# Performance work log

Measured on AMD Instinct MI355X. Metric: run time of the kernel, lower is better.

## Reference

```python
import jax, jax.numpy as jnp
import numpy as np

C_IN = 512


def _rms(h, gamma):
    # F.normalize(x, dim=1) * sqrt(C) * gamma  (channel_first, h: [b, c, l])
    c = h.shape[1]
    n = jnp.sqrt(jnp.sum(h * h, axis=1, keepdims=True))
    return h / jnp.maximum(n, 1e-12) * (c ** 0.5) * gamma[None, :, None]


def _pw(w, b, h):
    # 1x1 conv == pointwise linear over channel dim; h: [b, c, l]
    return jnp.einsum('oc,bcl->bol', w, h) + b[None, :, None]


def setup_inputs() -> dict:
    key = jax.random.key(0)
    ks = jax.random.split(key, 10)
    B, C, T, H, W = 1, C_IN, 16, 32, 32
    inp = {'x': jax.random.normal(ks[0], (B, C, T, H, W), jnp.float32)}
    names = ['qs', 'ks', 'vs', 'ps', 'qt', 'kt', 'vt', 'pt']
    for i, n in enumerate(names):
        inp[n + '_w'] = jax.random.normal(ks[i + 1], (C, C), jnp.float32) * 0.02
        inp[n + '_b'] = jnp.zeros((C,), jnp.float32)
    inp['norm_s_gamma'] = jnp.ones((C,), jnp.float32)
    inp['norm_t_gamma'] = jnp.ones((C,), jnp.float32)
    inp['max_temporal_window'] = 8
    return inp


def reference(x, qs_w, qs_b, ks_w, ks_b, vs_w, vs_b, ps_w, ps_b,
              qt_w, qt_b, kt_w, kt_b, vt_w, vt_b, pt_w, pt_b,
              norm_s_gamma, norm_t_gamma, max_temporal_window):
    B, C, T, H, W = x.shape
    scale = C ** -0.5

    # ---- spatial attention: (b t) c (h w) ----
    xs = x.transpose(0, 2, 1, 3, 4).reshape(B * T, C, H * W)
    h = _rms(xs, norm_s_gamma)
    q = _pw(qs_w, qs_b, h)
    k = _pw(ks_w, ks_b, h)
    v = _pw(vs_w, vs_b, h)
    scores = jnp.einsum('bcl,bcm->blm', q, k) * scale  # [bt, HW, HW]
    attn = jax.nn.softmax(scores, axis=-1)
    o = jnp.einsum('bcm,blm->bcl', v, attn)
    xs = xs + _pw(ps_w, ps_b, o)
    x = xs.reshape(B, T, C, H, W).transpose(0, 2, 1, 3, 4)

    # ---- temporal attention: (b h w) c t, causal + bounded window ----
    xt = x.transpose(0, 3, 4, 1, 2).reshape(B * H * W, C, T)
    h = _rms(xt, norm_t_gamma)
    q = _pw(qt_w, qt_b, h)
    k = _pw(kt_w, kt_b, h)
    v = _pw(vt_w, vt_b, h)
    scores = jnp.einsum('bcl,bcm->blm', q, k) * scale  # [bhw, T, T]
    i = jnp.arange(T)[:, None]
    j = jnp.arange(T)[None, :]
    allowed = j <= i  # causal
    if max_temporal_window is not None and max_temporal_window > 0:
        allowed = allowed & (i - j < max_temporal_window)  # sliding window
    mask = jnp.where(allowed, 0.0, jnp.finfo(scores.dtype).min)
    attn = jax.nn.softmax(scores + mask[None], axis=-1)
    o = jnp.einsum('bcm,blm->bcl', v, attn)
    xt = xt + _pw(pt_w, pt_b, o)
    x = xt.reshape(B, H, W, C, T).transpose(0, 3, 4, 1, 2)
    return x
```

## Files before the change

### kernel.cpp

```cpp
#include <hip/hip_runtime.h>

typedef __attribute__((ext_vector_type(8))) short bf16x8;
typedef __attribute__((ext_vector_type(4))) float f32x4;

__device__ __forceinline__ short f2bf(float f) {
  union { float f; unsigned u; } a; a.f = f;
  unsigned r = a.u + 0x7fffu + ((a.u >> 16) & 1u);
  return (short)(r >> 16);
}
__device__ __forceinline__ float bf2f(short s) {
  union { unsigned u; float f; } a;
  a.u = ((unsigned)(unsigned short)s) << 16; return a.f;
}
__device__ __forceinline__ float blo(unsigned u) { union { unsigned u; float f; } a; a.u = u << 16; return a.f; }
__device__ __forceinline__ float bhi(unsigned u) { union { unsigned u; float f; } a; a.u = u & 0xffff0000u; return a.f; }
__device__ __forceinline__ unsigned packbf(float lo, float hi) {
  return (unsigned)(unsigned short)f2bf(lo) | ((unsigned)(unsigned short)f2bf(hi) << 16);
}
__device__ __forceinline__ void ldscp16(const void* g, void* l) {
  __builtin_amdgcn_global_load_lds((const __attribute__((address_space(1))) void*)g,
                                   (__attribute__((address_space(3))) void*)l, 16, 0, 0);
}
__device__ __forceinline__ void stv(float* p, float v) { *p = v; }
__device__ __forceinline__ void stv(short* p, float v) { *p = f2bf(v); }

__global__ __launch_bounds__(256) void setup_all(
    const float* __restrict__ w0, const float* __restrict__ w1,
    const float* __restrict__ w2, const float* __restrict__ w3,
    const float* __restrict__ w4, const float* __restrict__ w5,
    const float* __restrict__ w6, const float* __restrict__ w7,
    const float* __restrict__ g_s, const float* __restrict__ g_t,
    short* __restrict__ Wb, float* __restrict__ zs,
    const float* __restrict__ qs_b, const float* __restrict__ vs_b,
    const float* __restrict__ ps_b, const float* __restrict__ qt_b,
    const float* __restrict__ vt_b, const float* __restrict__ pt_b,
    float* __restrict__ bt_s, float* __restrict__ bt_t,
    float* __restrict__ wus, float* __restrict__ wut) {
  const int bid = blockIdx.x, tid = threadIdx.x;
  if (bid < 8192) {
    int idx = bid * 256 + tid;
    const float* ws[8] = {w0, w1, w2, w3, w4, w5, w6, w7};
    int wi = idx >> 18, loc = idx & 262143;
    int r = loc >> 9, q = loc & 511;
    float v, g;
    if (wi == 3 || wi == 7) { v = ws[wi][loc]; g = 1.f; }
    else {
      v = ws[wi][q * 512 + r];
      g = (wi <= 2) ? g_s[r] : g_t[r];
    }
    Wb[idx] = f2bf(v * g);
  } else if (bid < 8512) {
    zs[(bid - 8192) * 256 + tid] = 0.f;
  } else {
    const int w = tid >> 6, lane = tid & 63;
    const int b = (bid - 8512) * 4 + w;
    float s = 0.f;
    if (b < 1024) {
      const bool sp = b < 512;
      const float* W = sp ? w3 : w7;
      const float* vb = sp ? vs_b : vt_b;
      const int r = b & 511;
#pragma unroll
      for (int c = lane; c < 512; c += 64) s += W[r * 512 + c] * vb[c];
#pragma unroll
      for (int off = 32; off > 0; off >>= 1) s += __shfl_xor(s, off);
      if (lane == 0) (sp ? bt_s : bt_t)[r] = s + (sp ? ps_b : pt_b)[r];
    } else {
      const bool sp = b < 1536;
      const float* W = sp ? w1 : w5;
      const float* qb = sp ? qs_b : qt_b;
      const int c = b & 511;
#pragma unroll
      for (int o = lane; o < 512; o += 64) s += W[o * 512 + c] * qb[o];
#pragma unroll
      for (int off = 32; off > 0; off >>= 1) s += __shfl_xor(s, off);
      if (lane == 0)
        (sp ? wus : wut)[c] = s * (sp ? g_s[c] : g_t[c]);
    }
  }
}

__global__ __launch_bounds__(256) void txp_sumsq(
    const float* __restrict__ src, short* __restrict__ dst,
    short* __restrict__ xb, float* __restrict__ ss,
    const float* __restrict__ wu, float* __restrict__ us) {
  constexpr long N = 16384;
  __shared__ short T[64][66];
  __shared__ float part[16][16][4];
  __shared__ float part2[16][16][4];
  const int tid = threadIdx.x;
  const long n0 = (long)blockIdx.x * 64;
  const int c0 = blockIdx.y * 64;
  const int n4 = (tid & 15) * 4;
  float s0 = 0.f, s1 = 0.f, s2 = 0.f, s3 = 0.f;
  float u0 = 0.f, u1 = 0.f, u2 = 0.f, u3 = 0.f;
#pragma unroll
  for (int i = 0; i < 4; ++i) {
    int cl = i * 16 + (tid >> 4);
    float4 v = *(const float4*)&src[(long)(c0 + cl) * N + n0 + n4];
    float wc = wu[c0 + cl];
    s0 += v.x * v.x; s1 += v.y * v.y; s2 += v.z * v.z; s3 += v.w * v.w;
    u0 += wc * v.x; u1 += wc * v.y; u2 += wc * v.z; u3 += wc * v.w;
    short e0 = f2bf(v.x), e1 = f2bf(v.y), e2 = f2bf(v.z), e3 = f2bf(v.w);
    T[n4 + 0][cl] = e0; T[n4 + 1][cl] = e1;
    T[n4 + 2][cl] = e2; T[n4 + 3][cl] = e3;
    uint2 o;
    o.x = (unsigned)(unsigned short)e0 | ((unsigned)(unsigned short)e1 << 16);
    o.y = (unsigned)(unsigned short)e2 | ((unsigned)(unsigned short)e3 << 16);
    *(uint2*)&xb[(long)(c0 + cl) * N + n0 + n4] = o;
  }
  part[tid >> 4][tid & 15][0] = s0; part[tid >> 4][tid & 15][1] = s1;
  part[tid >> 4][tid & 15][2] = s2; part[tid >> 4][tid & 15][3] = s3;
  part2[tid >> 4][tid & 15][0] = u0; part2[tid >> 4][tid & 15][1] = u1;
  part2[tid >> 4][tid & 15][2] = u2; part2[tid >> 4][tid & 15][3] = u3;
  __syncthreads();
  if (tid < 64) {
    float s = 0.f, u = 0.f;
#pragma unroll
    for (int cg = 0; cg < 16; ++cg) {
      s += part[cg][tid >> 2][tid & 3];
      u += part2[cg][tid >> 2][tid & 3];
    }
    atomicAdd(&ss[n0 + tid], s);
    atomicAdd(&us[n0 + tid], u);
  }
#pragma unroll
  for (int p = 0; p < 4; ++p) {
    int nl = p * 16 + (tid >> 4);
    int cl = (tid & 15) * 4;
    uint2 o;
    o.x = (unsigned)(unsigned short)T[nl][cl] |
          ((unsigned)(unsigned short)T[nl][cl + 1] << 16);
    o.y = (unsigned)(unsigned short)T[nl][cl + 2] |
          ((unsigned)(unsigned short)T[nl][cl + 3] << 16);
    *(uint2*)&dst[(n0 + nl) * 512 + c0 + cl] = o;
  }
}

template <typename OutT, int BIAS_MODE, int SCALE_MODE, int RESID_MODE, int EPI,
          int BM = 128, int FOLD = 0, int BK = 64, int SWZ = 0>
__global__ __launch_bounds__(256, (BM == 64) ? 5 : 4) void gemm_nt(
    const short* __restrict__ A, const short* __restrict__ B,
    OutT* __restrict__ D, const float* __restrict__ bias,
    const float* __restrict__ ssv, const float* __restrict__ uvec,
    float* __restrict__ rs, float* __restrict__ rs2,
    const float* __restrict__ wvec,
    const float* __restrict__ residf, const short* __restrict__ residb,
    int K, int lda, int ldb, int ldd,
    long aBatch, long bBatch, long dBatch, long sBatch, float scale) {
  constexpr int WR = (BM >= 64) ? BM / 64 : 1;
  constexpr int WC = 4 / WR;
  constexpr int NW = (128 / WC) / 16;
  constexpr int WCS = 128 / WC;
  constexpr int CH = BK / 8;
  constexpr int MSK = CH - 1;
  constexpr int RPR = 256 / CH;
  __shared__ short As[BM * BK];
  __shared__ short Bs[128 * BK];
  const int tid = threadIdx.x;

  int lin = blockIdx.x + gridDim.x * (blockIdx.y + gridDim.y * blockIdx.z);
  if (SWZ) {
    const int nwg = gridDim.x * gridDim.y * gridDim.z;
    const int q = nwg >> 3, r = nwg & 7;
    const int xcd = lin & 7, idx = lin >> 3;
    lin = (xcd < r ? xcd * (q + 1) : r * (q + 1) + (xcd - r) * q) + idx;
  }
  const int bx = lin % gridDim.x;
  const int t1 = lin / gridDim.x;
  const int by = t1 % gridDim.y;
  const int bz = t1 / gridDim.y;

  const long i0 = (long)bx * BM;
  const long j0 = (long)by * 128;
  long aOff, bOff;
  if (FOLD) {
    aOff = 262144L * (bz < 2 ? 3 + 4 * bz : 4 * (bz - 2));
    bOff = 262144L * (bz < 2 ? 2 + 4 * bz : 1 + 4 * (bz - 2));
  } else {
    aOff = bz * aBatch; bOff = bz * bBatch;
  }
  const short* Ab = A + aOff + i0 * lda;
  const short* Bb = B + bOff + j0 * ldb;
  const int srow = tid / CH, scol = tid & MSK;
  const int lane = tid & 63;
  const int waveid = tid >> 6;
  const int wr = (waveid / WC) * 64;
  const int wc = (waveid % WC) * WCS;
  const int quad = lane >> 4, l15 = lane & 15;

  f32x4 acc[4][NW] = {};

  for (int k0 = 0; k0 < K; k0 += BK) {
    __syncthreads();
#pragma unroll
    for (int p = 0; p < BM / RPR; ++p) {
      int row = p * RPR + srow;
      int gc = (scol ^ (row & MSK)) << 3;
      ldscp16(Ab + (long)row * lda + k0 + gc, &As[p * 2048 + tid * 8]);
    }
#pragma unroll
    for (int p = 0; p < 128 / RPR; ++p) {
      int row = p * RPR + srow;
      int gc = (scol ^ (row & MSK)) << 3;
      ldscp16(Bb + (long)row * ldb + k0 + gc, &Bs[p * 2048 + tid * 8]);
    }
    __syncthreads();
#pragma unroll
    for (int kk = 0; kk < BK / 32; ++kk) {
      bf16x8 af[4], bfr[NW];
#pragma unroll
      for (int a = 0; a < 4; ++a) {
        int row = wr + a * 16 + l15;
        int g = kk * 4 + quad;
        af[a] = *(const bf16x8*)&As[row * BK + ((g ^ (row & MSK)) << 3)];
      }
#pragma unroll
      for (int b = 0; b < NW; ++b) {
        int row = wc + b * 16 + l15;
        int g = kk * 4 + quad;
        bfr[b] = *(const bf16x8*)&Bs[row * BK + ((g ^ (row & MSK)) << 3)];
      }
#pragma unroll
      for (int a = 0; a < 4; ++a)
#pragma unroll
        for (int b = 0; b < NW; ++b)
          acc[a][b] = __builtin_amdgcn_mfma_f32_16x16x32_bf16(af[a], bfr[b], acc[a][b], 0, 0, 0);
    }
  }

  const long Doff = bz * dBatch;
#pragma unroll
  for (int a = 0; a < 4; ++a) {
    const int rb = (int)i0 + wr + a * 16 + quad * 4;
    float rsc[4];
    if (SCALE_MODE == 1 || SCALE_MODE == 4) {
#pragma unroll
      for (int r = 0; r < 4; ++r)
        rsc[r] = 22.627416997969522f /
                 fmaxf(sqrtf(ssv[bz * sBatch + rb + r]), 1e-12f);
    }
    if (SCALE_MODE == 3) {
#pragma unroll
      for (int r = 0; r < 4; ++r)
        rsc[r] = 1.f / ssv[bz * sBatch + rb + r];
    }
    float rp1[4] = {0.f, 0.f, 0.f, 0.f};
    float rp2[4] = {0.f, 0.f, 0.f, 0.f};
#pragma unroll
    for (int b = 0; b < NW; ++b) {
      const int cc = (int)j0 + wc + b * 16 + l15;
      float csc = 1.f, uu = 0.f, wv = 0.f;
      if (SCALE_MODE == 2 || SCALE_MODE == 4)
        csc = 22.627416997969522f /
              fmaxf(sqrtf(ssv[bz * sBatch + cc]), 1e-12f);
      if (SCALE_MODE == 4) uu = uvec[bz * sBatch + cc];
      if (EPI == 3) wv = wvec[cc];
      uint2 rtv;
      if (RESID_MODE == 3)
        rtv = *(const uint2*)&residb[(long)cc * 512 + rb];
#pragma unroll
      for (int r = 0; r < 4; ++r) {
        float val;
        if (SCALE_MODE == 4) {
          val = __expf(scale * csc * (rsc[r] * acc[a][b][r] + uu));
          rp1[r] += val;
          val *= csc;
        } else {
          val = acc[a][b][r] * scale;
          if (SCALE_MODE == 1 || SCALE_MODE == 3) val *= rsc[r];
          if (SCALE_MODE == 2) val *= csc;
        }
        if (BIAS_MODE == 1) val += bias[rb + r];
        if (BIAS_MODE == 2) val += bias[cc];
        const long off = Doff + (long)(rb + r) * ldd + cc;
        if (RESID_MODE == 1) val += residf[off];
        if (RESID_MODE == 2) val += bf2f(residb[off]);
        if (RESID_MODE == 3) val += bf2f(((const short*)&rtv)[r]);
        stv(D + off, val);
        if (EPI == 3) { rp1[r] += val * val; rp2[r] += val * wv; }
      }
    }
    if (EPI == 1 || EPI == 3) {
#pragma unroll
      for (int r = 0; r < 4; ++r) {
        float s = rp1[r];
#pragma unroll
        for (int off = 1; off < 16; off <<= 1) s += __shfl_xor(s, off);
        if (l15 == 0) atomicAdd(&rs[bz * sBatch + rb + r], s);
      }
      if (EPI == 3) {
#pragma unroll
        for (int r = 0; r < 4; ++r) {
          float s = rp2[r];
#pragma unroll
          for (int off = 1; off < 16; off <<= 1) s += __shfl_xor(s, off);
          if (l15 == 0) atomicAdd(&rs2[bz * sBatch + rb + r], s);
        }
      }
    }
  }
}

__global__ __launch_bounds__(256) void temporal_attn_v5(
    const short* __restrict__ h2, const short* __restrict__ Tt,
    const float* __restrict__ ss, const float* __restrict__ ut,
    const int* __restrict__ wndp, short* __restrict__ o, float scale) {
  constexpr int RS = 520;
  __shared__ short hq[16 * RS];
  __shared__ short tk[16 * RS];
  __shared__ float Plds[16][17];
  const int tid = threadIdx.x;
  const int w = tid >> 6, lane = tid & 63;
  const int hw = blockIdx.x;
  const int wnd = *wndp;

#pragma unroll
  for (int i = 0; i < 8; ++i) {
    int ci = w * 8 + i;
    int t = ci & 15;
    const short* src = (ci < 16) ? h2 : Tt;
    short* dst = (ci < 16) ? hq : tk;
    ldscp16(src + (long)(t * 1024 + hw) * 512 + lane * 8,
            dst + t * RS + lane * 8);
  }
  const int c0 = lane * 8;
  uint4 vch[16];
#pragma unroll
  for (int tp = 0; tp < 16; ++tp)
    vch[tp] = *(const uint4*)(h2 + (long)(tp * 1024 + hw) * 512 + c0);
  __syncthreads();

  if (w == 0) {
    const int quad = lane >> 4, m = lane & 15;
    f32x4 sacc = {};
#pragma unroll
    for (int s = 0; s < 16; ++s) {
      bf16x8 aq = *(const bf16x8*)&hq[m * RS + quad * 8 + s * 32];
      bf16x8 bk = *(const bf16x8*)&tk[m * RS + quad * 8 + s * 32];
      sacc = __builtin_amdgcn_mfma_f32_16x16x32_bf16(aq, bk, sacc, 0, 0, 0);
    }
    const float rmsj = 22.627416997969522f /
                       fmaxf(sqrtf(ss[m * 1024 + hw]), 1e-12f);
    const float uj = ut[m * 1024 + hw];
#pragma unroll
    for (int r = 0; r < 4; ++r) {
      const int i = quad * 4 + r;
      const int j = m;
      const float rmsi = 22.627416997969522f /
                         fmaxf(sqrtf(ss[i * 1024 + hw]), 1e-12f);
      const bool allowed = (j <= i) && (wnd <= 0 || (i - j) < wnd);
      float val = allowed ? scale * (rmsi * rmsj * sacc[r] + rmsj * uj) : -1e30f;
      float mx = val;
#pragma unroll
      for (int off = 1; off < 16; off <<= 1) mx = fmaxf(mx, __shfl_xor(mx, off));
      float e = allowed ? __expf(val - mx) : 0.f;
      float sum = e;
#pragma unroll
      for (int off = 1; off < 16; off <<= 1) sum += __shfl_xor(sum, off);
      Plds[i][j] = (e / sum) * rmsj;
    }
  }
  __syncthreads();

#pragma unroll
  for (int r = 0; r < 4; ++r) {
    const int t = w * 4 + r;
    const int tlo = (wnd > 0 && t - wnd + 1 > 0) ? t - wnd + 1 : 0;
    float a0 = 0.f, a1 = 0.f, a2 = 0.f, a3 = 0.f,
          a4 = 0.f, a5 = 0.f, a6 = 0.f, a7 = 0.f;
#pragma unroll
    for (int tp = 0; tp < 16; ++tp) {
      const float p = (tp >= tlo && tp <= t) ? Plds[t][tp] : 0.f;
      const uint4 vv = vch[tp];
      a0 += p * blo(vv.x); a1 += p * bhi(vv.x);
      a2 += p * blo(vv.y); a3 += p * bhi(vv.y);
      a4 += p * blo(vv.z); a5 += p * bhi(vv.z);
      a6 += p * blo(vv.w); a7 += p * bhi(vv.w);
    }
    uint4 ov;
    ov.x = packbf(a0, a1); ov.y = packbf(a2, a3);
    ov.z = packbf(a4, a5); ov.w = packbf(a6, a7);
    *(uint4*)(o + (long)(t * 1024 + hw) * 512 + c0) = ov;
  }
}

extern "C" void kernel_launch(void* const* d_in, const int* in_sizes, int n_in,
                              void* d_out, int out_size, void* d_ws, size_t ws_size,
                              hipStream_t stream) {
  const float* x    = (const float*)d_in[0];
  const float* qs_w = (const float*)d_in[1];
  const float* qs_b = (const float*)d_in[2];
  const float* ks_w = (const float*)d_in[3];
  const float* ks_b = (const float*)d_in[4];
  const float* vs_w = (const float*)d_in[5];
  const float* vs_b = (const float*)d_in[6];
  const float* ps_w = (const float*)d_in[7];
  const float* ps_b = (const float*)d_in[8];
  const float* qt_w = (const float*)d_in[9];
  const float* qt_b = (const float*)d_in[10];
  const float* kt_w = (const float*)d_in[11];
  const float* kt_b = (const float*)d_in[12];
  const float* vt_w = (const float*)d_in[13];
  const float* vt_b = (const float*)d_in[14];
  const float* pt_w = (const float*)d_in[15];
  const float* pt_b = (const float*)d_in[16];
  const float* g_s  = (const float*)d_in[17];
  const float* g_t  = (const float*)d_in[18];
  const int*   wnd  = (const int*)d_in[19];
  float* out = (float*)d_out;
  (void)ks_b; (void)kt_b;

  char* w = (char*)d_ws;
  short* Wb   = (short*)(w);
  float* ss_s = (float*)(w + (4L << 20));
  float* ss_t = (float*)(w + (4L << 20) + (64 << 10));
  float* rsum = (float*)(w + (4L << 20) + (128 << 10));
  float* us   = (float*)(w + (4L << 20) + (192 << 10));
  float* ut   = (float*)(w + (4L << 20) + (256 << 10));
  float* bt_s = (float*)(w + (4L << 20) + (320 << 10));
  float* bt_t = (float*)(w + (4L << 20) + (324 << 10));
  float* wus  = (float*)(w + (4L << 20) + (328 << 10));
  float* wut  = (float*)(w + (4L << 20) + (332 << 10));
  short* WF   = (short*)(w + (4L << 20) + (512 << 10));
  short* Wpv  = WF;
  short* Mqk  = WF + 2 * 262144;
  short* hb   = (short*)(w + (8L << 20));
  short* Tb   = (short*)(w + (24L << 20));
  short* xb   = (short*)(w + (40L << 20));
  short* oT   = (short*)(w + (56L << 20));
  short* h2   = (short*)(w + (72L << 20));
  short* S    = (short*)(w + (88L << 20));
  (void)in_sizes; (void)n_in; (void)out_size; (void)ws_size;

  const float scale = 0.04419417382415922f;

  setup_all<<<9024, 256, 0, stream>>>(
      qs_w, ks_w, vs_w, ps_w, qt_w, kt_w, vt_w, pt_w, g_s, g_t, Wb, ss_s,
      qs_b, vs_b, ps_b, qt_b, vt_b, pt_b, bt_s, bt_t, wus, wut);
  gemm_nt<short, 0, 0, 0, 0, 128, 1, 64, 0><<<dim3(4, 4, 4), 256, 0, stream>>>(
      Wb, Wb, WF, nullptr, nullptr, nullptr, nullptr, nullptr, nullptr,
      nullptr, nullptr, 512, 512, 512, 512, 0, 0, 262144L, 0, 1.f);

  txp_sumsq<<<dim3(256, 8, 1), 256, 0, stream>>>(x, hb, xb, ss_s, wus, us);
  gemm_nt<short, 0, 0, 0, 0, 64, 0, 64, 1><<<dim3(256, 4, 1), 256, 0, stream>>>(
      hb, Mqk, Tb, nullptr, nullptr, nullptr, nullptr, nullptr, nullptr,
      nullptr, nullptr, 512, 512, 512, 512, 0, 0, 0, 0, 1.f);
  gemm_nt<short, 0, 4, 0, 1, 64, 0, 64, 1><<<dim3(16, 8, 16), 256, 0, stream>>>(
      hb, Tb, S, nullptr, ss_s, us, rsum, nullptr, nullptr, nullptr, nullptr,
      512, 512, 512, 1024,
      1024L * 512, 1024L * 512, 1024L * 1024, 1024, scale);
  gemm_nt<short, 0, 3, 0, 0, 64, 0, 64, 1><<<dim3(16, 4, 16), 256, 0, stream>>>(
      S, xb, oT, nullptr, rsum, nullptr, nullptr, nullptr, nullptr,
      nullptr, nullptr, 1024, 1024, 16384, 512,
      1024L * 1024, 1024L, 1024L * 512, 1024, 1.f);
  gemm_nt<short, 2, 0, 2, 3, 64, 0, 64, 1><<<dim3(256, 4, 1), 256, 0, stream>>>(
      oT, Wpv, h2, bt_s, nullptr, nullptr, ss_t, ut, wut, nullptr, hb,
      512, 512, 512, 512, 0, 0, 0, 1024, 1.f);

  gemm_nt<short, 0, 0, 0, 0, 64, 0, 64, 1><<<dim3(256, 4, 1), 256, 0, stream>>>(
      h2, Mqk + 262144, Tb, nullptr, nullptr, nullptr, nullptr, nullptr,
      nullptr, nullptr, nullptr, 512, 512, 512, 512, 0, 0, 0, 0, 1.f);
  temporal_attn_v5<<<1024, 256, 0, stream>>>(h2, Tb, ss_t, ut, wnd, oT, scale);
  gemm_nt<float, 1, 0, 3, 0, 64, 0, 64, 1><<<dim3(8, 128, 1), 256, 0, stream>>>(
      Wpv + 262144, oT, out, bt_t, nullptr, nullptr, nullptr, nullptr,
      nullptr, nullptr, h2, 512, 512, 512, 16384, 0, 0, 0, 0, 1.f);
}
```

Baseline: 300.5 us.

## Generalize GEMM tiling and use wide 32xN tiles with full-row B reuse

The GEMM template is parameterized by BM, BN, warp layout and min-blocks. Most projection and attention GEMMs now use 32-row tiles that span the full N (512 or 1024), so each A tile is loaded once per block instead of once per N-tile. The inner loop is reordered to load one B fragment at a time, which reduces register pressure. The wide tiles increase LDS and register use and cut occupancy (launch-bounds min-blocks 2), and the 1024-wide score GEMM also uses BK=32.

```diff
diff --git a/kernel.cpp b/kernel.cpp
--- a/kernel.cpp
+++ b/kernel.cpp
@@ -138,8 +138,8 @@
 }
 
 template <typename OutT, int BIAS_MODE, int SCALE_MODE, int RESID_MODE, int EPI,
-          int BM = 128, int FOLD = 0, int BK = 64, int SWZ = 0>
-__global__ __launch_bounds__(256, (BM == 64) ? 5 : 4) void gemm_nt(
+          int BM, int BN, int BK, int WR, int WC, int FOLD, int SWZ, int MINB>
+__global__ __launch_bounds__(256, MINB) void gemm_nt(
     const short* __restrict__ A, const short* __restrict__ B,
     OutT* __restrict__ D, const float* __restrict__ bias,
     const float* __restrict__ ssv, const float* __restrict__ uvec,
@@ -148,15 +148,16 @@
     const float* __restrict__ residf, const short* __restrict__ residb,
     int K, int lda, int ldb, int ldd,
     long aBatch, long bBatch, long dBatch, long sBatch, float scale) {
-  constexpr int WR = (BM >= 64) ? BM / 64 : 1;
-  constexpr int WC = 4 / WR;
-  constexpr int NW = (128 / WC) / 16;
-  constexpr int WCS = 128 / WC;
+  constexpr int MR = BM / WR / 16;
+  constexpr int NW = BN / WC / 16;
+  constexpr int WRS = BM / WR;
+  constexpr int WCS = BN / WC;
   constexpr int CH = BK / 8;
   constexpr int MSK = CH - 1;
-  constexpr int RPR = 256 / CH;
+  constexpr int ACH = BM * CH;
+  constexpr int BCH = BN * CH;
   __shared__ short As[BM * BK];
-  __shared__ short Bs[128 * BK];
+  __shared__ short Bs[BN * BK];
   const int tid = threadIdx.x;
 
   int lin = blockIdx.x + gridDim.x * (blockIdx.y + gridDim.y * blockIdx.z);
@@ -172,7 +173,7 @@
   const int bz = t1 / gridDim.y;
 
   const long i0 = (long)bx * BM;
-  const long j0 = (long)by * 128;
+  const long j0 = (long)by * BN;
   long aOff, bOff;
   if (FOLD) {
     aOff = 262144L * (bz < 2 ? 3 + 4 * bz : 4 * (bz - 2));
@@ -182,35 +183,40 @@
   }
   const short* Ab = A + aOff + i0 * lda;
   const short* Bb = B + bOff + j0 * ldb;
-  const int srow = tid / CH, scol = tid & MSK;
   const int lane = tid & 63;
   const int waveid = tid >> 6;
-  const int wr = (waveid / WC) * 64;
+  const int wr = (waveid / WC) * WRS;
   const int wc = (waveid % WC) * WCS;
   const int quad = lane >> 4, l15 = lane & 15;
 
-  f32x4 acc[4][NW] = {};
+  f32x4 acc[MR][NW] = {};
 
   for (int k0 = 0; k0 < K; k0 += BK) {
     __syncthreads();
 #pragma unroll
-    for (int p = 0; p < BM / RPR; ++p) {
-      int row = p * RPR + srow;
-      int gc = (scol ^ (row & MSK)) << 3;
-      ldscp16(Ab + (long)row * lda + k0 + gc, &As[p * 2048 + tid * 8]);
-    }
-#pragma unroll
-    for (int p = 0; p < 128 / RPR; ++p) {
-      int row = p * RPR + srow;
-      int gc = (scol ^ (row & MSK)) << 3;
-      ldscp16(Bb + (long)row * ldb + k0 + gc, &Bs[p * 2048 + tid * 8]);
+    for (int p = 0; p < (ACH + 255) / 256; ++p) {
+      int idx = p * 256 + tid;
+      if ((ACH & 255) == 0 || idx < ACH) {
+        int row = idx / CH, sc = idx & MSK;
+        ldscp16(Ab + (long)row * lda + k0 + ((sc ^ (row & MSK)) << 3),
+                &As[idx * 8]);
+      }
+    }
+#pragma unroll
+    for (int p = 0; p < (BCH + 255) / 256; ++p) {
+      int idx = p * 256 + tid;
+      if ((BCH & 255) == 0 || idx < BCH) {
+        int row = idx / CH, sc = idx & MSK;
+        ldscp16(Bb + (long)row * ldb + k0 + ((sc ^ (row & MSK)) << 3),
+                &Bs[idx * 8]);
+      }
     }
     __syncthreads();
 #pragma unroll
     for (int kk = 0; kk < BK / 32; ++kk) {
-      bf16x8 af[4], bfr[NW];
-#pragma unroll
-      for (int a = 0; a < 4; ++a) {
+      bf16x8 af[MR];
+#pragma unroll
+      for (int a = 0; a < MR; ++a) {
         int row = wr + a * 16 + l15;
         int g = kk * 4 + quad;
         af[a] = *(const bf16x8*)&As[row * BK + ((g ^ (row & MSK)) << 3)];
@@ -219,19 +225,17 @@
       for (int b = 0; b < NW; ++b) {
         int row = wc + b * 16 + l15;
         int g = kk * 4 + quad;
-        bfr[b] = *(const bf16x8*)&Bs[row * BK + ((g ^ (row & MSK)) << 3)];
-      }
-#pragma unroll
-      for (int a = 0; a < 4; ++a)
-#pragma unroll
-        for (int b = 0; b < NW; ++b)
-          acc[a][b] = __builtin_amdgcn_mfma_f32_16x16x32_bf16(af[a], bfr[b], acc[a][b], 0, 0, 0);
+        bf16x8 bf = *(const bf16x8*)&Bs[row * BK + ((g ^ (row & MSK)) << 3)];
+#pragma unroll
+        for (int a = 0; a < MR; ++a)
+          acc[a][b] = __builtin_amdgcn_mfma_f32_16x16x32_bf16(af[a], bf, acc[a][b], 0, 0, 0);
+      }
     }
   }
 
   const long Doff = bz * dBatch;
 #pragma unroll
-  for (int a = 0; a < 4; ++a) {
+  for (int a = 0; a < MR; ++a) {
     const int rb = (int)i0 + wr + a * 16 + quad * 4;
     float rsc[4];
     if (SCALE_MODE == 1 || SCALE_MODE == 4) {
@@ -438,31 +442,38 @@
   setup_all<<<9024, 256, 0, stream>>>(
       qs_w, ks_w, vs_w, ps_w, qt_w, kt_w, vt_w, pt_w, g_s, g_t, Wb, ss_s,
       qs_b, vs_b, ps_b, qt_b, vt_b, pt_b, bt_s, bt_t, wus, wut);
-  gemm_nt<short, 0, 0, 0, 0, 128, 1, 64, 0><<<dim3(4, 4, 4), 256, 0, stream>>>(
+  gemm_nt<short, 0, 0, 0, 0, 128, 128, 64, 2, 2, 1, 0, 4>
+      <<<dim3(4, 4, 4), 256, 0, stream>>>(
       Wb, Wb, WF, nullptr, nullptr, nullptr, nullptr, nullptr, nullptr,
       nullptr, nullptr, 512, 512, 512, 512, 0, 0, 262144L, 0, 1.f);
 
   txp_sumsq<<<dim3(256, 8, 1), 256, 0, stream>>>(x, hb, xb, ss_s, wus, us);
-  gemm_nt<short, 0, 0, 0, 0, 64, 0, 64, 1><<<dim3(256, 4, 1), 256, 0, stream>>>(
+  gemm_nt<short, 0, 0, 0, 0, 32, 512, 64, 1, 4, 0, 1, 2>
+      <<<dim3(512, 1, 1), 256, 0, stream>>>(
       hb, Mqk, Tb, nullptr, nullptr, nullptr, nullptr, nullptr, nullptr,
       nullptr, nullptr, 512, 512, 512, 512, 0, 0, 0, 0, 1.f);
-  gemm_nt<short, 0, 4, 0, 1, 64, 0, 64, 1><<<dim3(16, 8, 16), 256, 0, stream>>>(
+  gemm_nt<short, 0, 4, 0, 1, 32, 1024, 32, 1, 4, 0, 1, 2>
+      <<<dim3(32, 1, 16), 256, 0, stream>>>(
       hb, Tb, S, nullptr, ss_s, us, rsum, nullptr, nullptr, nullptr, nullptr,
       512, 512, 512, 1024,
       1024L * 512, 1024L * 512, 1024L * 1024, 1024, scale);
-  gemm_nt<short, 0, 3, 0, 0, 64, 0, 64, 1><<<dim3(16, 4, 16), 256, 0, stream>>>(
+  gemm_nt<short, 0, 3, 0, 0, 32, 512, 64, 1, 4, 0, 1, 2>
+      <<<dim3(32, 1, 16), 256, 0, stream>>>(
       S, xb, oT, nullptr, rsum, nullptr, nullptr, nullptr, nullptr,
       nullptr, nullptr, 1024, 1024, 16384, 512,
       1024L * 1024, 1024L, 1024L * 512, 1024, 1.f);
-  gemm_nt<short, 2, 0, 2, 3, 64, 0, 64, 1><<<dim3(256, 4, 1), 256, 0, stream>>>(
+  gemm_nt<short, 2, 0, 2, 3, 32, 512, 64, 1, 4, 0, 1, 2>
+      <<<dim3(512, 1, 1), 256, 0, stream>>>(
       oT, Wpv, h2, bt_s, nullptr, nullptr, ss_t, ut, wut, nullptr, hb,
       512, 512, 512, 512, 0, 0, 0, 1024, 1.f);
 
-  gemm_nt<short, 0, 0, 0, 0, 64, 0, 64, 1><<<dim3(256, 4, 1), 256, 0, stream>>>(
+  gemm_nt<short, 0, 0, 0, 0, 32, 512, 64, 1, 4, 0, 1, 2>
+      <<<dim3(512, 1, 1), 256, 0, stream>>>(
       h2, Mqk + 262144, Tb, nullptr, nullptr, nullptr, nullptr, nullptr,
       nullptr, nullptr, nullptr, 512, 512, 512, 512, 0, 0, 0, 0, 1.f);
   temporal_attn_v5<<<1024, 256, 0, stream>>>(h2, Tb, ss_t, ut, wnd, oT, scale);
-  gemm_nt<float, 1, 0, 3, 0, 64, 0, 64, 1><<<dim3(8, 128, 1), 256, 0, stream>>>(
+  gemm_nt<float, 1, 0, 3, 0, 128, 128, 64, 2, 2, 0, 1, 4>
+      <<<dim3(4, 128, 1), 256, 0, stream>>>(
       Wpv + 262144, oT, out, bt_t, nullptr, nullptr, nullptr, nullptr,
       nullptr, nullptr, h2, 512, 512, 512, 16384, 0, 0, 0, 0, 1.f);
 }
```

New measurement: 323.7 us. +7.7%, slower.
